# Kernel tuning notes

Hardware: AMD Instinct MI355X
Metric: run time of the kernel (lower is better)

Reference implementation:

```python
import jax, jax.numpy as jnp
import numpy as np

THR = 1.0     # snntorch Leaky default threshold
BETA = 0.9    # args.beta
ALPHA = 2.0   # surrogate.atan default alpha

@jax.custom_vjp
def atan_spike(x):
    # Heaviside forward, arctan surrogate gradient (snntorch surrogate.atan)
    return (x > 0).astype(x.dtype)

def _aspk_fwd(x):
    return atan_spike(x), x

def _aspk_bwd(x, g):
    return (g * (ALPHA / 2.0) / (1.0 + (jnp.pi / 2.0 * ALPHA * x) ** 2),)

atan_spike.defvjp(_aspk_fwd, _aspk_bwd)

def setup_inputs() -> dict:
    key = jax.random.key(0)
    k = jax.random.split(key, 5)
    B, D, H, C = 32768, 187, 50, 5
    return {
        "x": jax.random.normal(k[0], (B, D), dtype=jnp.float32),
        "W1": jax.random.normal(k[1], (H, D), dtype=jnp.float32) * (1.0 / np.sqrt(D)),
        "b1": jax.random.normal(k[2], (H,), dtype=jnp.float32) * 0.01,
        "W2": jax.random.normal(k[3], (C, H), dtype=jnp.float32) * (1.0 / np.sqrt(H)),
        "b2": jax.random.normal(k[4], (C,), dtype=jnp.float32) * 0.01,
        "num_steps": 100,
    }

def reference(x, W1, b1, W2, b2, num_steps):
    B = x.shape[0]
    dt = x.dtype
    # fc1(x) is identical every timestep (x is static), compute once
    cur1 = x @ W1.T + b1  # [B, 50]

    def step(carry, _):
        mem1, mem2 = carry
        # Leaky: reset computed from PREVIOUS mem (detached), subtract mechanism
        reset1 = jax.lax.stop_gradient((mem1 > THR).astype(dt))
        mem1 = BETA * mem1 + cur1 - reset1 * THR
        spk1 = atan_spike(mem1 - THR)
        cur2 = spk1 @ W2.T + b2  # [B, num_classes]
        reset2 = jax.lax.stop_gradient((mem2 > THR).astype(dt))
        mem2 = BETA * mem2 + cur2 - reset2 * THR
        spk2 = atan_spike(mem2 - THR)
        return (mem1, mem2), (spk2, mem2)

    init = (jnp.zeros((B, W1.shape[0]), dt), jnp.zeros((B, W2.shape[0]), dt))
    _, (spk_rec, mem_rec) = jax.lax.scan(step, init, None, length=num_steps)
    return spk_rec, mem_rec  # each [num_steps, B, num_classes]
```

## Files before the change

### kernel.cpp

```cpp
#include <hip/hip_runtime.h>

typedef float v2f __attribute__((ext_vector_type(2)));
typedef float v4f __attribute__((ext_vector_type(4)));

#define DD   187
#define HH   50
#define PH   64
#define HPJ  8
#define NP   4
#define NC   5
#define RPB  32
#define BLK  256
#define DCH  64
#define NCHUNK 3
#define XSS  68
#define BETA 0.9f

__device__ __forceinline__ float dpp_xor1(float v) {
    return __builtin_bit_cast(float,
        __builtin_amdgcn_mov_dpp(__builtin_bit_cast(int, v), 0xB1, 0xF, 0xF, true));
}
__device__ __forceinline__ float dpp_xor2(float v) {
    return __builtin_bit_cast(float,
        __builtin_amdgcn_mov_dpp(__builtin_bit_cast(int, v), 0x4E, 0xF, 0xF, true));
}
__device__ __forceinline__ float dpp_xor8(float v) {
    return __builtin_bit_cast(float,
        __builtin_amdgcn_mov_dpp(__builtin_bit_cast(int, v), 0x128, 0xF, 0xF, true));
}

__device__ __forceinline__ float spike1(float m) {
    float t = fmaf(m, 0x1.0p60f, -0x1.0p60f);
    return fminf(fmaxf(t, 0.f), 1.f);
}
__device__ __forceinline__ v2f spike2(v2f m) {
    const v2f BIG2  = { 0x1.0p60f,  0x1.0p60f};
    const v2f NBIG2 = {-0x1.0p60f, -0x1.0p60f};
    const v2f ONE2  = {1.f, 1.f};
    const v2f ZERO2 = {0.f, 0.f};
    v2f t = __builtin_elementwise_fma(m, BIG2, NBIG2);
    return __builtin_elementwise_min(__builtin_elementwise_max(t, ZERO2), ONE2);
}

__global__ __launch_bounds__(BLK, 4)
void snn_kernel(const float* __restrict__ x,
                const float* __restrict__ W1,
                const float* __restrict__ b1,
                const float* __restrict__ W2,
                const float* __restrict__ b2,
                const int*   __restrict__ nsp,
                float* __restrict__ out, int Brows)
{
    __shared__ float xs[RPB * XSS];
    __shared__ float w1t[DCH * PH];

    const int tid = threadIdx.x;
    const int l   = tid & 15;
    const int g   = tid >> 4;
    const int hb  = (l >> 2) & 1;
    const int p   = g * 2 + hb;
    const int k   = (l & 3) | ((l & 8) >> 1);
    const int row = blockIdx.x * RPB + p;
    const int NS  = nsp[0];

    v2f acc[NP];
#pragma unroll
    for (int i = 0; i < NP; ++i) acc[i] = (v2f){0.f, 0.f};

    for (int ch = 0; ch < NCHUNK; ++ch) {
        const int d0 = ch * DCH;
        for (int i = tid; i < RPB * DCH; i += BLK) {
            int r = i >> 6, dd = i & 63;
            int d = d0 + dd;
            xs[r * XSS + dd] = (d < DD) ? x[(size_t)(blockIdx.x * RPB + r) * DD + d] : 0.f;
        }
        for (int i = tid; i < DCH * PH; i += BLK) {
            int dd = i >> 6, h = i & 63;
            int d = d0 + dd;
            w1t[dd * PH + h] = (h < HH && d < DD) ? W1[h * DD + d] : 0.f;
        }
        __syncthreads();

        const float* xr = xs + p * XSS;
#pragma unroll 4
        for (int d4 = 0; d4 < DCH / 4; ++d4) {
            v4f xv4 = *(const v4f*)(xr + 4 * d4);
#pragma unroll
            for (int j = 0; j < 4; ++j) {
                int d = 4 * d4 + j;
                const v4f* wr = (const v4f*)(w1t + d * PH + k * HPJ);
                v4f wa = wr[0], wb = wr[1];
                float xv = xv4[j];
                v2f xvv = {xv, xv};
                acc[0] = __builtin_elementwise_fma(xvv, __builtin_shufflevector(wa, wa, 0, 1), acc[0]);
                acc[1] = __builtin_elementwise_fma(xvv, __builtin_shufflevector(wa, wa, 2, 3), acc[1]);
                acc[2] = __builtin_elementwise_fma(xvv, __builtin_shufflevector(wb, wb, 0, 1), acc[2]);
                acc[3] = __builtin_elementwise_fma(xvv, __builtin_shufflevector(wb, wb, 2, 3), acc[3]);
            }
        }
        __syncthreads();
    }

    v2f c1[NP];
#pragma unroll
    for (int i = 0; i < NP; ++i) {
        int h0 = k * HPJ + 2 * i;
        v2f bb;
        bb.x = (h0     < HH) ? b1[h0]     : 0.f;
        bb.y = (h0 + 1 < HH) ? b1[h0 + 1] : 0.f;
        c1[i] = acc[i] + bb;
    }
    if (k == 7) c1[3].y = 2.0f;

    v2f w2r[NC][NP];
#pragma unroll
    for (int c = 0; c < NC; ++c)
#pragma unroll
        for (int i = 0; i < NP; ++i) {
            int h0 = k * HPJ + 2 * i;
            w2r[c][i].x = (h0     < HH) ? W2[c * HH + h0]     : 0.f;
            w2r[c][i].y = (h0 + 1 < HH) ? W2[c * HH + h0 + 1] : 0.f;
        }
    if (k == 7) {
#pragma unroll
        for (int c = 0; c < NC; ++c) w2r[c][3].y = b2[c];
    }

    v2f m1[NP], s1[NP];
#pragma unroll
    for (int i = 0; i < NP; ++i) { m1[i] = (v2f){0.f, 0.f}; s1[i] = (v2f){0.f, 0.f}; }
    float mA = 0.f, sA = 0.f;

    const size_t stride = (size_t)Brows * NC;
    float* spkBase = out;
    float* memBase = out + (size_t)NS * stride;
    const int offA = row * NC + k;
    const bool owner = (k < NC);
    const v2f BETA2 = {BETA, BETA};

    for (int t = 0; t < NS; ++t) {
        v2f cp[NC];
#pragma unroll
        for (int c = 0; c < NC; ++c) cp[c] = (v2f){0.f, 0.f};
#pragma unroll
        for (int i = 0; i < NP; ++i) {
            v2f m = __builtin_elementwise_fma(BETA2, m1[i], c1[i]) - s1[i];
            m1[i] = m;
            v2f s = spike2(m);
            s1[i] = s;
#pragma unroll
            for (int c = 0; c < NC; ++c)
                cp[c] = __builtin_elementwise_fma(s, w2r[c][i], cp[c]);
        }
        float cur2[NC];
#pragma unroll
        for (int c = 0; c < NC; ++c) {
            float r = cp[c].x + cp[c].y;
            r += dpp_xor1(r);
            r += dpp_xor2(r);
            r += dpp_xor8(r);
            cur2[c] = r;
        }
        float cA = (k == 1) ? cur2[1] : (k == 2) ? cur2[2] :
                   (k == 3) ? cur2[3] : (k == 4) ? cur2[4] : cur2[0];

        mA = fmaf(BETA, mA, cA) - sA;
        sA = spike1(mA);

        if (owner) {
            spkBase[offA] = sA;
            memBase[offA] = mA;
        }
        spkBase += stride;
        memBase += stride;
    }
}

extern "C" void kernel_launch(void* const* d_in, const int* in_sizes, int n_in,
                              void* d_out, int out_size, void* d_ws, size_t ws_size,
                              hipStream_t stream) {
    const float* x  = (const float*)d_in[0];
    const float* W1 = (const float*)d_in[1];
    const float* b1 = (const float*)d_in[2];
    const float* W2 = (const float*)d_in[3];
    const float* b2 = (const float*)d_in[4];
    const int*   ns = (const int*)d_in[5];
    int B = in_sizes[0] / DD;
    int nblocks = B / RPB;
    snn_kernel<<<nblocks, BLK, 0, stream>>>(x, W1, b1, W2, b2, ns, (float*)d_out, B);
}
```

Measured before the change: 232.4 us.

## Use 4 threads per row with 14 hidden units each and software-pipeline timestep

Changes the thread mapping so each batch row is handled by 4 lanes owning 14 hidden units each, rather than 8 lanes with 8 units, and doubles rows per block to 64. The cross-lane reduction drops to two DPP steps, and the layer-1 update for the next timestep is issued before the output update of the current one to overlap the dependency chain. This needs more registers per thread, so occupancy is pinned to 2 waves per EU, and lane 0 now writes the fifth class output.

New measurement: 223.2 us. -4.0%, faster.

```diff
diff --git a/kernel.cpp b/kernel.cpp
--- a/kernel.cpp
+++ b/kernel.cpp
@@ -6,10 +6,11 @@
 #define DD   187
 #define HH   50
 #define PH   64
-#define HPJ  8
-#define NP   4
+#define HPJ  14
+#define HPL  16
+#define NP   7
 #define NC   5
-#define RPB  32
+#define RPB  64
 #define BLK  256
 #define DCH  64
 #define NCHUNK 3
@@ -23,10 +24,6 @@
 __device__ __forceinline__ float dpp_xor2(float v) {
     return __builtin_bit_cast(float,
         __builtin_amdgcn_mov_dpp(__builtin_bit_cast(int, v), 0x4E, 0xF, 0xF, true));
-}
-__device__ __forceinline__ float dpp_xor8(float v) {
-    return __builtin_bit_cast(float,
-        __builtin_amdgcn_mov_dpp(__builtin_bit_cast(int, v), 0x128, 0xF, 0xF, true));
 }
 
 __device__ __forceinline__ float spike1(float m) {
@@ -42,7 +39,10 @@
     return __builtin_elementwise_min(__builtin_elementwise_max(t, ZERO2), ONE2);
 }
 
-__global__ __launch_bounds__(BLK, 4)
+__device__ __forceinline__ v2f vlo(v4f v) { return __builtin_shufflevector(v, v, 0, 1); }
+__device__ __forceinline__ v2f vhi(v4f v) { return __builtin_shufflevector(v, v, 2, 3); }
+
+__global__ __launch_bounds__(BLK) __attribute__((amdgpu_waves_per_eu(2, 2)))
 void snn_kernel(const float* __restrict__ x,
                 const float* __restrict__ W1,
                 const float* __restrict__ b1,
@@ -51,15 +51,12 @@
                 const int*   __restrict__ nsp,
                 float* __restrict__ out, int Brows)
 {
-    __shared__ float xs[RPB * XSS];
-    __shared__ float w1t[DCH * PH];
+    __shared__ __align__(16) float xs[RPB * XSS];
+    __shared__ __align__(16) float w1t[DCH * PH];
 
     const int tid = threadIdx.x;
-    const int l   = tid & 15;
-    const int g   = tid >> 4;
-    const int hb  = (l >> 2) & 1;
-    const int p   = g * 2 + hb;
-    const int k   = (l & 3) | ((l & 8) >> 1);
+    const int p   = tid >> 2;
+    const int k   = tid & 3;
     const int row = blockIdx.x * RPB + p;
     const int NS  = nsp[0];
 
@@ -75,27 +72,35 @@
             xs[r * XSS + dd] = (d < DD) ? x[(size_t)(blockIdx.x * RPB + r) * DD + d] : 0.f;
         }
         for (int i = tid; i < DCH * PH; i += BLK) {
-            int dd = i >> 6, h = i & 63;
+            int dd = i >> 6, s = i & 63;
+            int kk = s >> 4, j = s & 15;
+            int h = kk * HPJ + j;
             int d = d0 + dd;
-            w1t[dd * PH + h] = (h < HH && d < DD) ? W1[h * DD + d] : 0.f;
+            w1t[dd * PH + s] = (j < HPJ && h < HH && d < DD) ? W1[h * DD + d] : 0.f;
         }
         __syncthreads();
 
         const float* xr = xs + p * XSS;
-#pragma unroll 4
+#pragma unroll 2
         for (int d4 = 0; d4 < DCH / 4; ++d4) {
             v4f xv4 = *(const v4f*)(xr + 4 * d4);
 #pragma unroll
             for (int j = 0; j < 4; ++j) {
                 int d = 4 * d4 + j;
-                const v4f* wr = (const v4f*)(w1t + d * PH + k * HPJ);
-                v4f wa = wr[0], wb = wr[1];
+                const float* wbase = w1t + d * PH + k * HPL;
+                v4f w0 = *(const v4f*)(wbase);
+                v4f w1v = *(const v4f*)(wbase + 4);
+                v4f w2v = *(const v4f*)(wbase + 8);
+                v2f w3 = *(const v2f*)(wbase + 12);
                 float xv = xv4[j];
                 v2f xvv = {xv, xv};
-                acc[0] = __builtin_elementwise_fma(xvv, __builtin_shufflevector(wa, wa, 0, 1), acc[0]);
-                acc[1] = __builtin_elementwise_fma(xvv, __builtin_shufflevector(wa, wa, 2, 3), acc[1]);
-                acc[2] = __builtin_elementwise_fma(xvv, __builtin_shufflevector(wb, wb, 0, 1), acc[2]);
-                acc[3] = __builtin_elementwise_fma(xvv, __builtin_shufflevector(wb, wb, 2, 3), acc[3]);
+                acc[0] = __builtin_elementwise_fma(xvv, vlo(w0),  acc[0]);
+                acc[1] = __builtin_elementwise_fma(xvv, vhi(w0),  acc[1]);
+                acc[2] = __builtin_elementwise_fma(xvv, vlo(w1v), acc[2]);
+                acc[3] = __builtin_elementwise_fma(xvv, vhi(w1v), acc[3]);
+                acc[4] = __builtin_elementwise_fma(xvv, vlo(w2v), acc[4]);
+                acc[5] = __builtin_elementwise_fma(xvv, vhi(w2v), acc[5]);
+                acc[6] = __builtin_elementwise_fma(xvv, w3,       acc[6]);
             }
         }
         __syncthreads();
@@ -110,7 +115,7 @@
         bb.y = (h0 + 1 < HH) ? b1[h0 + 1] : 0.f;
         c1[i] = acc[i] + bb;
     }
-    if (k == 7) c1[3].y = 2.0f;
+    if (k == 3) c1[6].y = 2.0f;
 
     v2f w2r[NC][NP];
 #pragma unroll
@@ -121,25 +126,25 @@
             w2r[c][i].x = (h0     < HH) ? W2[c * HH + h0]     : 0.f;
             w2r[c][i].y = (h0 + 1 < HH) ? W2[c * HH + h0 + 1] : 0.f;
         }
-    if (k == 7) {
-#pragma unroll
-        for (int c = 0; c < NC; ++c) w2r[c][3].y = b2[c];
+    if (k == 3) {
+#pragma unroll
+        for (int c = 0; c < NC; ++c) w2r[c][6].y = b2[c];
     }
 
     v2f m1[NP], s1[NP];
 #pragma unroll
     for (int i = 0; i < NP; ++i) { m1[i] = (v2f){0.f, 0.f}; s1[i] = (v2f){0.f, 0.f}; }
-    float mA = 0.f, sA = 0.f;
+    float mA = 0.f, sA = 0.f, mB = 0.f, sB = 0.f;
 
     const size_t stride = (size_t)Brows * NC;
     float* spkBase = out;
     float* memBase = out + (size_t)NS * stride;
     const int offA = row * NC + k;
-    const bool owner = (k < NC);
+    const int offB = row * NC + 4;
     const v2f BETA2 = {BETA, BETA};
 
-    for (int t = 0; t < NS; ++t) {
-        v2f cp[NC];
+    v2f cp[NC];
+    auto S1 = [&]() {
 #pragma unroll
         for (int c = 0; c < NC; ++c) cp[c] = (v2f){0.f, 0.f};
 #pragma unroll
@@ -152,25 +157,33 @@
             for (int c = 0; c < NC; ++c)
                 cp[c] = __builtin_elementwise_fma(s, w2r[c][i], cp[c]);
         }
+    };
+
+    S1();
+    for (int t = 0; t < NS; ++t) {
         float cur2[NC];
 #pragma unroll
         for (int c = 0; c < NC; ++c) {
             float r = cp[c].x + cp[c].y;
             r += dpp_xor1(r);
             r += dpp_xor2(r);
-            r += dpp_xor8(r);
             cur2[c] = r;
         }
+        S1();
+
         float cA = (k == 1) ? cur2[1] : (k == 2) ? cur2[2] :
-                   (k == 3) ? cur2[3] : (k == 4) ? cur2[4] : cur2[0];
+                   (k == 3) ? cur2[3] : cur2[0];
+        float cB = cur2[4];
 
         mA = fmaf(BETA, mA, cA) - sA;
         sA = spike1(mA);
-
-        if (owner) {
-            spkBase[offA] = sA;
-            memBase[offA] = mA;
-        }
+        mB = fmaf(BETA, mB, cB) - sB;
+        sB = spike1(mB);
+
+        spkBase[offA] = sA;
+        memBase[offA] = mA;
+        if (k == 0) { spkBase[offB] = sB; memBase[offB] = mB; }
+
         spkBase += stride;
         memBase += stride;
     }
```
